# Kernel tuning notes

Hardware: AMD Instinct MI355X
Metric: run time of the kernel (lower is better)

Reference implementation:

```python
import jax, jax.numpy as jnp
import numpy as np

B, S, H, D = 2, 512, 64, 64   # batch, seq_len, head_dim, d_v=d_k
DT = 0.01                      # uniform measurement time step
NU, DELTA, ETA = 0.5, 1.0, 1.0


def _cmat(k, dout, din, scale):
    kr, ki = jax.random.split(k)
    return jnp.stack([jax.random.normal(kr, (dout, din)),
                      jax.random.normal(ki, (dout, din))]) * scale


def _cmm(W, b, X):
    """Complex matmul + bias. W:(2,O,I), b:(2,O,1), X:(B,2,S,I) -> (B,2,S,O)."""
    Yr = X[:, 0] @ W[0].T - X[:, 1] @ W[1].T + b[0].T
    Yi = X[:, 0] @ W[1].T + X[:, 1] @ W[0].T + b[1].T
    return jnp.stack([Yr, Yi], axis=1)


def _chad(K, V):
    """Complex hadamard of kernel K:(2,Si,Sj,D) with V:(B,2,Sj,D) -> (B,2,Si,Sj,D)."""
    Vr, Vi = V[:, 0, None], V[:, 1, None]           # (B,1,Sj,D)
    return jnp.stack([K[0][None] * Vr - K[1][None] * Vi,
                      K[0][None] * Vi + K[1][None] * Vr], axis=1)


def setup_inputs() -> dict:
    key = jax.random.key(0)
    ks = jax.random.split(key, 20)
    sc = 1.0 / np.sqrt(2 * H)
    t = jnp.arange(S + 1, dtype=jnp.float32) * DT
    return {
        "X_q": jax.random.normal(ks[0], (B, 2, S, H), jnp.float32),
        "X_k": jax.random.normal(ks[1], (B, 2, S, H), jnp.float32),
        "X_v": jax.random.normal(ks[2], (B, 2, S, H), jnp.float32),
        "t_measure_all": jnp.tile(t[None], (B, 1)),
        "lambda1": jnp.stack([jax.random.normal(ks[3], (D // 2, 1)),
                              jax.random.normal(ks[4], (D // 2, 1))]),
        "lam_Omega_sqrt": jax.random.normal(ks[5], (1, D, 1)) / np.sqrt(D),
        "lam_Omega0_sqrt": jax.random.normal(ks[6], (1, D, 1)) / np.sqrt(D),
        "lam_Gamma_sqrt": jax.random.normal(ks[7], (1, D, 1)) / np.sqrt(D),
        "lam_C": jnp.ones((1, D, 1), jnp.float32),
        "W_q": _cmat(ks[8], D, H, sc), "W_k": _cmat(ks[9], D, H, sc),
        "W_v": _cmat(ks[10], D, H, sc), "W_p": _cmat(ks[11], H, D, sc),
        "W_e": _cmat(ks[12], H, D, sc),
        "b_q": _cmat(ks[13], D, 1, sc), "b_k": _cmat(ks[14], D, 1, sc),
        "b_v": _cmat(ks[15], D, 1, sc), "b_p": _cmat(ks[16], H, 1, sc),
        "b_e": _cmat(ks[17], H, 1, sc),
    }


def reference(X_q, X_k, X_v, t_measure_all, lambda1, lam_Omega_sqrt,
              lam_Omega0_sqrt, lam_Gamma_sqrt, lam_C, W_q, W_k, W_v, W_p, W_e,
              b_q, b_k, b_v, b_p, b_e):
    # Stable conjugate-pair eigenvalues lambda_h (real<0) from lambda1 (2, D/2, 1)
    lr = -jnp.abs(lambda1[0, :, 0])
    li = lambda1[1, :, 0]
    real = jnp.concatenate([lr, lr])        # (D,)
    imag = jnp.concatenate([li, -li])       # (D,)
    Om = (lam_Omega_sqrt ** 2)[0, :, 0]
    Om0 = (lam_Omega0_sqrt ** 2)[0, :, 0]
    Gam = (lam_Gamma_sqrt ** 2)[0, :, 0]
    C = lam_C[0, :, 0]

    # Complex QKV projections
    Q = _cmm(W_q, b_q, X_q)
    Kk = _cmm(W_k, b_k, X_k)
    V = _cmm(W_v, b_v, X_v)

    # Pairwise propagation kernel exp(lambda * (t_i - t_j))
    t = t_measure_all[0, :-1]                       # (S,)
    dt = t[:, None] - t[None, :]                    # (S,S)
    decay = jnp.exp(real * dt[:, :, None])
    ph = imag * dt[:, :, None]
    Kexp = jnp.stack([decay * jnp.cos(ph), decay * jnp.sin(ph)])  # (2,S,S,D)

    # Kalman steady-state precision: propagated variance + measurement noise
    exp2 = jnp.exp((2.0 * real) * jnp.abs(dt)[:, :, None])        # (S,S,D)
    var = exp2 * Om0 + Om * (exp2 - 1.0) / (2.0 * real)
    P = 1.0 / (C ** 2 * var + Gam)                                # (S,S,D)

    # Estimates (propagated values) and residuals (query vs propagated key)
    Xhat = _chad(Kexp, V)                           # (B,2,S,S,D)
    Khat = _chad(Kexp, Kk)
    R = Q[:, :, :, None, :] - C * Khat              # (B,2,S,S,D)

    maha = P * (R[:, 0] ** 2 + R[:, 1] ** 2)        # (B,S,S,D)
    denom = 1.0 + NU * jnp.sum(maha, axis=-1, keepdims=True)
    mask = jnp.tril(jnp.ones((S, S), X_q.dtype))[:, :, None]
    A = (P / denom) * mask
    Xhat = Xhat * mask
    Qij = A / jnp.sum(A, axis=2, keepdims=True)     # normalize over j
    est_v = jnp.sum(Qij[:, None] * Xhat, axis=3)    # (B,2,S,D)

    est = _cmm(W_e, b_e, est_v)

    # One-step prediction in eigenbasis
    dtl = t_measure_all[:, -1] - t_measure_all[:, -2]   # (B,)
    dr = jnp.exp(real * dtl[:, None])
    pph = imag * dtl[:, None]
    mr, mi = dr * jnp.cos(pph), dr * jnp.sin(pph)       # (B,D)
    pr = mr[:, None] * est_v[:, 0] - mi[:, None] * est_v[:, 1]
    pi = mr[:, None] * est_v[:, 1] + mi[:, None] * est_v[:, 0]
    pred = _cmm(W_p, b_p, jnp.stack([pr, pi], axis=1))

    out = DELTA * pred + ETA * est
    return (est, out, Qij, Xhat, jnp.stack([real, imag]))
```

## Files before the change

### kernel.cpp

```cpp
#include <hip/hip_runtime.h>
#include <math.h>

#define SQ 512
#define NU_C 0.5f

typedef float fvec4 __attribute__((ext_vector_type(4)));

#define EST_OFF   0
#define OUT_OFF   131072
#define QIJ_OFF   262144
#define XHAT_OFF  33816576
#define LAM_OFF   100925440

#define WQ_OFF  0
#define WK_OFF  131072
#define WV_OFF  262144
#define WEV_OFF 393216

__global__ __launch_bounds__(256) void proj_kernel(
    const float* __restrict__ Xq, const float* __restrict__ Xk, const float* __restrict__ Xv,
    const float* __restrict__ Wq, const float* __restrict__ Wk, const float* __restrict__ Wv,
    const float* __restrict__ bq, const float* __restrict__ bk, const float* __restrict__ bv,
    float* __restrict__ ws)
{
    const int TILE = 16;
    __shared__ float WT0[64 * 65];
    __shared__ float WT1[64 * 65];
    __shared__ float XT[2 * TILE * 64];

    int t   = threadIdx.x;
    int blk = blockIdx.x;
    int p   = blk >> 6;
    int sub = blk & 63;
    int b   = sub >> 5;
    int s0  = (sub & 31) * TILE;

    const float* Xs[3]   = {Xq, Xk, Xv};
    const float* Wsrc[3] = {Wq, Wk, Wv};
    const float* bs[3]   = {bq, bk, bv};
    float* dst[3] = {ws + WQ_OFF, ws + WK_OFF, ws + WV_OFF};

    const float* W = Wsrc[p];
    for (int it = 0; it < 16; ++it) {
        int e = it * 256 + t;
        int dd = e >> 6, hw = e & 63;
        WT0[hw * 65 + dd] = W[e];
        WT1[hw * 65 + dd] = W[4096 + e];
    }
    const float* X = Xs[p];
    for (int it = 0; it < (2 * TILE * 64) / 256; ++it) {
        int e = it * 256 + t;
        int ri = e >> 10;
        int sl = (e >> 6) & (TILE - 1);
        int hw = e & 63;
        XT[e] = X[(size_t)(b * 2 + ri) * (SQ * 64) + (size_t)(s0 + sl) * 64 + hw];
    }
    __syncthreads();

    int dd = t & 63, sg = t >> 6;
    float b0 = bs[p][dd], b1 = bs[p][64 + dd];
    for (int sl = sg; sl < TILE; sl += 4) {
        float ar = b0, ai = b1;
        for (int h = 0; h < 64; ++h) {
            float xr = XT[sl * 64 + h];
            float xi = XT[TILE * 64 + sl * 64 + h];
            float w0 = WT0[h * 65 + dd];
            float w1 = WT1[h * 65 + dd];
            ar += xr * w0 - xi * w1;
            ai += xr * w1 + xi * w0;
        }
        float2 o; o.x = ar; o.y = ai;
        *(float2*)&dst[p][(size_t)((b * SQ + s0 + sl) * 64 + dd) * 2] = o;
    }
}

__global__ __launch_bounds__(512, 4) void main_kernel(
    const float* __restrict__ tm,
    const float* __restrict__ lam1,
    const float* __restrict__ lOm, const float* __restrict__ lOm0,
    const float* __restrict__ lGam, const float* __restrict__ lC,
    const float* __restrict__ ws,
    float* __restrict__ evw,
    float* __restrict__ out)
{
    __shared__ float t_lds[SQ];
    __shared__ float rden_l[2][SQ];
    __shared__ float red[8][2][3][64];

    int tid  = threadIdx.x;
    int lane = tid & 63;
    int wave = tid >> 6;
    int d = lane;
    int bx = (int)blockIdx.x;
    int i = (bx < 256) ? (SQ - 1 - bx) : (bx - 256);

    float l0 = lam1[d & 31];
    float l1 = lam1[32 + (d & 31)];
    float realv = -fabsf(l0);
    float imagv = (d < 32) ? l1 : -l1;
    float Om  = lOm[d]  * lOm[d];
    float Om0 = lOm0[d] * lOm0[d];
    float Gam = lGam[d] * lGam[d];
    float C   = lC[d];
    float C2  = C * C;
    float r2r = 1.0f / (2.0f * realv);
    float pA  = C2 * (Om0 + Om * r2r);
    float pB  = Gam - C2 * Om * r2r;

    for (int q = tid; q < SQ; q += 512) t_lds[q] = tm[q];
    __syncthreads();

    const float2* Kw = (const float2*)(ws + WK_OFF);
    const float2* Vw = (const float2*)(ws + WV_OFF);
    const float2* Qw = (const float2*)(ws + WQ_OFF);

    float ti = t_lds[i];
    float2 q0 = Qw[(0 * SQ + i) * 64 + d];
    float2 q1 = Qw[(1 * SQ + i) * 64 + d];
    float sA0 = 0, sXr0 = 0, sXi0 = 0, sA1 = 0, sXr1 = 0, sXi1 = 0;

    float* xh0 = out + XHAT_OFF + (size_t)(0 * SQ + i) * SQ * 64;
    float* xh1 = out + XHAT_OFF + (size_t)(1 * SQ + i) * SQ * 64;
    float* xh2 = out + XHAT_OFF + (size_t)(2 * SQ + i) * SQ * 64;
    float* xh3 = out + XHAT_OFF + (size_t)(3 * SQ + i) * SQ * 64;
    float* qij0 = out + QIJ_OFF + (size_t)(0 * SQ + i) * SQ * 64;
    float* qij1 = out + QIJ_OFF + (size_t)(1 * SQ + i) * SQ * 64;

    #pragma unroll 2
    for (int j = wave; j <= i; j += 8) {
        float dt = ti - t_lds[j];
        float e = __expf(realv * dt);
        float sph, cph;
        __sincosf(imagv * dt, &sph, &cph);
        float ar = e * cph, ai = e * sph;
        float e2 = e * e;
        float P = 1.0f / fmaf(e2, pA, pB);

        float2 k0 = Kw[(0 * SQ + j) * 64 + d];
        float2 v0 = Vw[(0 * SQ + j) * 64 + d];
        float2 k1 = Kw[(1 * SQ + j) * 64 + d];
        float2 v1 = Vw[(1 * SQ + j) * 64 + d];

        float xr0 = ar * v0.x - ai * v0.y, xi0 = ar * v0.y + ai * v0.x;
        float xr1 = ar * v1.x - ai * v1.y, xi1 = ar * v1.y + ai * v1.x;
        float khr0 = ar * k0.x - ai * k0.y, khi0 = ar * k0.y + ai * k0.x;
        float khr1 = ar * k1.x - ai * k1.y, khi1 = ar * k1.y + ai * k1.x;
        float Rr0 = q0.x - C * khr0, Ri0 = q0.y - C * khi0;
        float Rr1 = q1.x - C * khr1, Ri1 = q1.y - C * khi1;
        float m0 = P * fmaf(Rr0, Rr0, Ri0 * Ri0);
        float m1 = P * fmaf(Rr1, Rr1, Ri1 * Ri1);
        #pragma unroll
        for (int off = 32; off > 0; off >>= 1) {
            m0 += __shfl_xor(m0, off);
            m1 += __shfl_xor(m1, off);
        }
        float rd0 = 1.0f / (1.0f + NU_C * m0);
        float rd1 = 1.0f / (1.0f + NU_C * m1);
        float A0 = P * rd0, A1 = P * rd1;
        sA0 += A0; sXr0 = fmaf(A0, xr0, sXr0); sXi0 = fmaf(A0, xi0, sXi0);
        sA1 += A1; sXr1 = fmaf(A1, xr1, sXr1); sXi1 = fmaf(A1, xi1, sXi1);

        size_t jb = (size_t)j * 64 + d;
        __builtin_nontemporal_store(xr0, xh0 + jb);
        __builtin_nontemporal_store(xi0, xh1 + jb);
        __builtin_nontemporal_store(xr1, xh2 + jb);
        __builtin_nontemporal_store(xi1, xh3 + jb);
        if (lane == 0) { rden_l[0][j] = rd0; rden_l[1][j] = rd1; }
    }
    red[wave][0][0][d] = sA0; red[wave][0][1][d] = sXr0; red[wave][0][2][d] = sXi0;
    red[wave][1][0][d] = sA1; red[wave][1][1][d] = sXr1; red[wave][1][2][d] = sXi1;
    __syncthreads();

    float tA0 = 0, tXr0 = 0, tXi0 = 0, tA1 = 0, tXr1 = 0, tXi1 = 0;
    #pragma unroll
    for (int w = 0; w < 8; ++w) {
        tA0 += red[w][0][0][d]; tXr0 += red[w][0][1][d]; tXi0 += red[w][0][2][d];
        tA1 += red[w][1][0][d]; tXr1 += red[w][1][1][d]; tXi1 += red[w][1][2][d];
    }
    float rs0 = 1.0f / tA0, rs1 = 1.0f / tA1;
    if (wave == 0) {
        float2 ev0; ev0.x = tXr0 * rs0; ev0.y = tXi0 * rs0;
        float2 ev1; ev1.x = tXr1 * rs1; ev1.y = tXi1 * rs1;
        *(float2*)&evw[(size_t)((0 * SQ + i) * 64 + d) * 2] = ev0;
        *(float2*)&evw[(size_t)((1 * SQ + i) * 64 + d) * 2] = ev1;
    }

    #pragma unroll 2
    for (int j = wave; j <= i; j += 8) {
        float dt = ti - t_lds[j];
        float e2 = __expf(2.0f * realv * dt);
        float P = 1.0f / fmaf(e2, pA, pB);
        float qv0 = P * rden_l[0][j] * rs0;
        float qv1 = P * rden_l[1][j] * rs1;
        size_t jb = (size_t)j * 64 + d;
        __builtin_nontemporal_store(qv0, qij0 + jb);
        __builtin_nontemporal_store(qv1, qij1 + jb);
    }

    int nz4 = ((SQ - 1 - i) * 64) >> 2;
    if (nz4 > 0) {
        fvec4 z = {0.f, 0.f, 0.f, 0.f};
        size_t zb = (size_t)(i + 1) * 64;
        float* regs[6] = {qij0 + zb, qij1 + zb, xh0 + zb, xh1 + zb, xh2 + zb, xh3 + zb};
        for (int r6 = 0; r6 < 6; ++r6) {
            float* p4 = regs[r6];
            for (int k4 = tid; k4 < nz4; k4 += 512)
                __builtin_nontemporal_store(z, (fvec4*)(p4 + (size_t)k4 * 4));
        }
    }
}

__global__ __launch_bounds__(256) void epi_kernel(
    const float* __restrict__ tm,
    const float* __restrict__ lam1,
    const float* __restrict__ We, const float* __restrict__ be,
    const float* __restrict__ Wp, const float* __restrict__ bp,
    const float* __restrict__ evw,
    float* __restrict__ out)
{
    const int TILE = 8;
    __shared__ float WT0[64 * 65];
    __shared__ float WT1[64 * 65];
    __shared__ float EVr[TILE * 64];
    __shared__ float EVi[TILE * 64];
    __shared__ float mr_s[64], mi_s[64];

    int t = threadIdx.x;
    int blk = blockIdx.x;
    int b = blk >> 6;
    int s0 = (blk & 63) * TILE;

    if (blk == 0 && t < 128) {
        int dd = t & 63;
        float l0 = lam1[dd & 31];
        float l1 = lam1[32 + (dd & 31)];
        float v = (t < 64) ? -fabsf(l0) : ((dd < 32) ? l1 : -l1);
        out[LAM_OFF + t] = v;
    }
    if (t < 64) {
        int dd = t;
        float l0 = lam1[dd & 31];
        float l1 = lam1[32 + (dd & 31)];
        float realv = -fabsf(l0);
        float imagv = (dd < 32) ? l1 : -l1;
        float dtl = tm[b * (SQ + 1) + SQ] - tm[b * (SQ + 1) + SQ - 1];
        float e = __expf(realv * dtl);
        float s, c; __sincosf(imagv * dtl, &s, &c);
        mr_s[dd] = e * c; mi_s[dd] = e * s;
    }
    {
        const float* src = evw + (size_t)(b * SQ + s0) * 128;
        for (int it = 0; it < (TILE * 128) / 256; ++it) {
            int e = it * 256 + t;
            float v = src[e];
            int sl = e >> 7, dd = (e >> 1) & 63, ri = e & 1;
            if (ri == 0) EVr[sl * 64 + dd] = v; else EVi[sl * 64 + dd] = v;
        }
    }
    for (int it = 0; it < 16; ++it) {
        int e = it * 256 + t;
        int hw = e >> 6, dd = e & 63;
        WT0[dd * 65 + hw] = We[e];
        WT1[dd * 65 + hw] = We[4096 + e];
    }
    __syncthreads();

    int h = t & 63, sg = t >> 6;
    float estr[2], esti[2];
    float be0 = be[h], be1 = be[64 + h];
    #pragma unroll
    for (int k = 0; k < 2; ++k) {
        int sl = sg + k * 4;
        float ar = be0, ai = be1;
        for (int dd = 0; dd < 64; ++dd) {
            float er = EVr[sl * 64 + dd], ei = EVi[sl * 64 + dd];
            float w0 = WT0[dd * 65 + h], w1 = WT1[dd * 65 + h];
            ar += er * w0 - ei * w1;
            ai += er * w1 + ei * w0;
        }
        estr[k] = ar; esti[k] = ai;
        out[EST_OFF + (size_t)((b * 2 + 0) * SQ + s0 + sl) * 64 + h] = ar;
        out[EST_OFF + (size_t)((b * 2 + 1) * SQ + s0 + sl) * 64 + h] = ai;
    }
    __syncthreads();
    for (int it = 0; it < 16; ++it) {
        int e = it * 256 + t;
        int hw = e >> 6, dd = e & 63;
        WT0[dd * 65 + hw] = Wp[e];
        WT1[dd * 65 + hw] = Wp[4096 + e];
    }
    __syncthreads();
    float bp0 = bp[h], bp1 = bp[64 + h];
    #pragma unroll
    for (int k = 0; k < 2; ++k) {
        int sl = sg + k * 4;
        float ar = bp0, ai = bp1;
        for (int dd = 0; dd < 64; ++dd) {
            float er = EVr[sl * 64 + dd], ei = EVi[sl * 64 + dd];
            float pr = mr_s[dd] * er - mi_s[dd] * ei;
            float pi = mr_s[dd] * ei + mi_s[dd] * er;
            float w0 = WT0[dd * 65 + h], w1 = WT1[dd * 65 + h];
            ar += pr * w0 - pi * w1;
            ai += pr * w1 + pi * w0;
        }
        out[OUT_OFF + (size_t)((b * 2 + 0) * SQ + s0 + sl) * 64 + h] = ar + estr[k];
        out[OUT_OFF + (size_t)((b * 2 + 1) * SQ + s0 + sl) * 64 + h] = ai + esti[k];
    }
}

extern "C" void kernel_launch(void* const* d_in, const int* in_sizes, int n_in,
                              void* d_out, int out_size, void* d_ws, size_t ws_size,
                              hipStream_t stream)
{
    const float* Xq   = (const float*)d_in[0];
    const float* Xk   = (const float*)d_in[1];
    const float* Xv   = (const float*)d_in[2];
    const float* tm   = (const float*)d_in[3];
    const float* lam1 = (const float*)d_in[4];
    const float* lOm  = (const float*)d_in[5];
    const float* lOm0 = (const float*)d_in[6];
    const float* lGam = (const float*)d_in[7];
    const float* lC   = (const float*)d_in[8];
    const float* Wq   = (const float*)d_in[9];
    const float* Wk   = (const float*)d_in[10];
    const float* Wv   = (const float*)d_in[11];
    const float* Wp   = (const float*)d_in[12];
    const float* We   = (const float*)d_in[13];
    const float* bq   = (const float*)d_in[14];
    const float* bk   = (const float*)d_in[15];
    const float* bv   = (const float*)d_in[16];
    const float* bp   = (const float*)d_in[17];
    const float* be   = (const float*)d_in[18];
    float* out = (float*)d_out;
    float* ws  = (float*)d_ws;

    proj_kernel<<<192, 256, 0, stream>>>(Xq, Xk, Xv, Wq, Wk, Wv, bq, bk, bv, ws);
    main_kernel<<<512, 512, 0, stream>>>(tm, lam1, lOm, lOm0, lGam, lC, ws, ws + WEV_OFF, out);
    epi_kernel<<<128, 256, 0, stream>>>(tm, lam1, We, be, Wp, bp, ws + WEV_OFF, out);
}
```

Measured before the change: 113.5 us.

## Process two j rows per wave with two d lanes per thread

Remaps the main kernel so each wave handles two key rows j at once (half-waves of 32 lanes), with each lane covering two adjacent d values. This allows 16-byte vector loads of K/V/Q and 8-byte vector stores of Xhat/Qij, and shortens the cross-lane reduction to 5 shuffle steps. It also moves the final reduction to wave 0 and broadcasts the reciprocal sums through shared memory. The costs are an extra barrier, a per-iteration bounds check with possible half-wave idling, and higher register pressure.

Result: no change. 112.3 us (median of 2 runs) (-1.1%).

```diff
diff --git a/kernel.cpp b/kernel.cpp
--- a/kernel.cpp
+++ b/kernel.cpp
@@ -5,6 +5,7 @@
 #define NU_C 0.5f
 
 typedef float fvec4 __attribute__((ext_vector_type(4)));
+typedef float fvec2 __attribute__((ext_vector_type(2)));
 
 #define EST_OFF   0
 #define OUT_OFF   131072
@@ -86,38 +87,45 @@
     __shared__ float t_lds[SQ];
     __shared__ float rden_l[2][SQ];
     __shared__ float red[8][2][3][64];
+    __shared__ float rs_l[2][64];
 
     int tid  = threadIdx.x;
     int lane = tid & 63;
     int wave = tid >> 6;
-    int d = lane;
+    int q    = lane & 31;
+    int h2   = lane >> 5;
+    int d0   = 2 * q, d1 = 2 * q + 1;
     int bx = (int)blockIdx.x;
     int i = (bx < 256) ? (SQ - 1 - bx) : (bx - 256);
 
-    float l0 = lam1[d & 31];
-    float l1 = lam1[32 + (d & 31)];
-    float realv = -fabsf(l0);
-    float imagv = (d < 32) ? l1 : -l1;
-    float Om  = lOm[d]  * lOm[d];
-    float Om0 = lOm0[d] * lOm0[d];
-    float Gam = lGam[d] * lGam[d];
-    float C   = lC[d];
-    float C2  = C * C;
-    float r2r = 1.0f / (2.0f * realv);
-    float pA  = C2 * (Om0 + Om * r2r);
-    float pB  = Gam - C2 * Om * r2r;
-
-    for (int q = tid; q < SQ; q += 512) t_lds[q] = tm[q];
-    __syncthreads();
-
-    const float2* Kw = (const float2*)(ws + WK_OFF);
-    const float2* Vw = (const float2*)(ws + WV_OFF);
-    const float2* Qw = (const float2*)(ws + WQ_OFF);
+    float la0 = lam1[d0 & 31], lb0 = lam1[32 + (d0 & 31)];
+    float la1 = lam1[d1 & 31], lb1 = lam1[32 + (d1 & 31)];
+    float rv0 = -fabsf(la0),  rv1 = -fabsf(la1);
+    float iv0 = (d0 < 32) ? lb0 : -lb0;
+    float iv1 = (d1 < 32) ? lb1 : -lb1;
+    float Om_0 = lOm[d0] * lOm[d0],   Om_1 = lOm[d1] * lOm[d1];
+    float Oo_0 = lOm0[d0] * lOm0[d0], Oo_1 = lOm0[d1] * lOm0[d1];
+    float Gm_0 = lGam[d0] * lGam[d0], Gm_1 = lGam[d1] * lGam[d1];
+    float C_0 = lC[d0], C_1 = lC[d1];
+    float r2r0 = 1.0f / (2.0f * rv0), r2r1 = 1.0f / (2.0f * rv1);
+    float pA0 = C_0 * C_0 * (Oo_0 + Om_0 * r2r0);
+    float pB0 = Gm_0 - C_0 * C_0 * Om_0 * r2r0;
+    float pA1 = C_1 * C_1 * (Oo_1 + Om_1 * r2r1);
+    float pB1 = Gm_1 - C_1 * C_1 * Om_1 * r2r1;
+
+    for (int s = tid; s < SQ; s += 512) t_lds[s] = tm[s];
+    __syncthreads();
+
+    const fvec4* Kw4 = (const fvec4*)(ws + WK_OFF);
+    const fvec4* Vw4 = (const fvec4*)(ws + WV_OFF);
+    const fvec4* Qw4 = (const fvec4*)(ws + WQ_OFF);
 
     float ti = t_lds[i];
-    float2 q0 = Qw[(0 * SQ + i) * 64 + d];
-    float2 q1 = Qw[(1 * SQ + i) * 64 + d];
-    float sA0 = 0, sXr0 = 0, sXi0 = 0, sA1 = 0, sXr1 = 0, sXi1 = 0;
+    fvec4 qb0 = Qw4[(size_t)(0 * SQ + i) * 32 + q];
+    fvec4 qb1 = Qw4[(size_t)(1 * SQ + i) * 32 + q];
+
+    float sA00 = 0, sA01 = 0, sXr00 = 0, sXr01 = 0, sXi00 = 0, sXi01 = 0;
+    float sA10 = 0, sA11 = 0, sXr10 = 0, sXr11 = 0, sXi10 = 0, sXi11 = 0;
 
     float* xh0 = out + XHAT_OFF + (size_t)(0 * SQ + i) * SQ * 64;
     float* xh1 = out + XHAT_OFF + (size_t)(1 * SQ + i) * SQ * 64;
@@ -127,74 +135,114 @@
     float* qij1 = out + QIJ_OFF + (size_t)(1 * SQ + i) * SQ * 64;
 
     #pragma unroll 2
-    for (int j = wave; j <= i; j += 8) {
-        float dt = ti - t_lds[j];
-        float e = __expf(realv * dt);
-        float sph, cph;
-        __sincosf(imagv * dt, &sph, &cph);
-        float ar = e * cph, ai = e * sph;
-        float e2 = e * e;
-        float P = 1.0f / fmaf(e2, pA, pB);
-
-        float2 k0 = Kw[(0 * SQ + j) * 64 + d];
-        float2 v0 = Vw[(0 * SQ + j) * 64 + d];
-        float2 k1 = Kw[(1 * SQ + j) * 64 + d];
-        float2 v1 = Vw[(1 * SQ + j) * 64 + d];
-
-        float xr0 = ar * v0.x - ai * v0.y, xi0 = ar * v0.y + ai * v0.x;
-        float xr1 = ar * v1.x - ai * v1.y, xi1 = ar * v1.y + ai * v1.x;
-        float khr0 = ar * k0.x - ai * k0.y, khi0 = ar * k0.y + ai * k0.x;
-        float khr1 = ar * k1.x - ai * k1.y, khi1 = ar * k1.y + ai * k1.x;
-        float Rr0 = q0.x - C * khr0, Ri0 = q0.y - C * khi0;
-        float Rr1 = q1.x - C * khr1, Ri1 = q1.y - C * khi1;
-        float m0 = P * fmaf(Rr0, Rr0, Ri0 * Ri0);
-        float m1 = P * fmaf(Rr1, Rr1, Ri1 * Ri1);
+    for (int j0 = 2 * wave; j0 <= i; j0 += 16) {
+        int j = j0 + h2;
+        if (j <= i) {
+            float dt = ti - t_lds[j];
+            float e_0 = __expf(rv0 * dt);
+            float e_1 = __expf(rv1 * dt);
+            float s_0, c_0, s_1, c_1;
+            __sincosf(iv0 * dt, &s_0, &c_0);
+            __sincosf(iv1 * dt, &s_1, &c_1);
+            float ar0 = e_0 * c_0, ai0 = e_0 * s_0;
+            float ar1 = e_1 * c_1, ai1 = e_1 * s_1;
+            float P_0 = 1.0f / fmaf(e_0 * e_0, pA0, pB0);
+            float P_1 = 1.0f / fmaf(e_1 * e_1, pA1, pB1);
+
+            fvec4 k0 = Kw4[(size_t)(0 * SQ + j) * 32 + q];
+            fvec4 v0 = Vw4[(size_t)(0 * SQ + j) * 32 + q];
+            fvec4 k1 = Kw4[(size_t)(1 * SQ + j) * 32 + q];
+            fvec4 v1 = Vw4[(size_t)(1 * SQ + j) * 32 + q];
+
+            float xr00 = ar0 * v0[0] - ai0 * v0[1], xi00 = ar0 * v0[1] + ai0 * v0[0];
+            float xr01 = ar1 * v0[2] - ai1 * v0[3], xi01 = ar1 * v0[3] + ai1 * v0[2];
+            float kr00 = ar0 * k0[0] - ai0 * k0[1], ki00 = ar0 * k0[1] + ai0 * k0[0];
+            float kr01 = ar1 * k0[2] - ai1 * k0[3], ki01 = ar1 * k0[3] + ai1 * k0[2];
+            float Rr00 = qb0[0] - C_0 * kr00, Ri00 = qb0[1] - C_0 * ki00;
+            float Rr01 = qb0[2] - C_1 * kr01, Ri01 = qb0[3] - C_1 * ki01;
+            float xr10 = ar0 * v1[0] - ai0 * v1[1], xi10 = ar0 * v1[1] + ai0 * v1[0];
+            float xr11 = ar1 * v1[2] - ai1 * v1[3], xi11 = ar1 * v1[3] + ai1 * v1[2];
+            float kr10 = ar0 * k1[0] - ai0 * k1[1], ki10 = ar0 * k1[1] + ai0 * k1[0];
+            float kr11 = ar1 * k1[2] - ai1 * k1[3], ki11 = ar1 * k1[3] + ai1 * k1[2];
+            float Rr10 = qb1[0] - C_0 * kr10, Ri10 = qb1[1] - C_0 * ki10;
+            float Rr11 = qb1[2] - C_1 * kr11, Ri11 = qb1[3] - C_1 * ki11;
+
+            float m0 = P_0 * fmaf(Rr00, Rr00, Ri00 * Ri00) + P_1 * fmaf(Rr01, Rr01, Ri01 * Ri01);
+            float m1 = P_0 * fmaf(Rr10, Rr10, Ri10 * Ri10) + P_1 * fmaf(Rr11, Rr11, Ri11 * Ri11);
+            #pragma unroll
+            for (int off = 16; off > 0; off >>= 1) {
+                m0 += __shfl_xor(m0, off);
+                m1 += __shfl_xor(m1, off);
+            }
+            float rdb0 = 1.0f / (1.0f + NU_C * m0);
+            float rdb1 = 1.0f / (1.0f + NU_C * m1);
+            float A00 = P_0 * rdb0, A01 = P_1 * rdb0;
+            float A10 = P_0 * rdb1, A11 = P_1 * rdb1;
+            sA00 += A00; sXr00 = fmaf(A00, xr00, sXr00); sXi00 = fmaf(A00, xi00, sXi00);
+            sA01 += A01; sXr01 = fmaf(A01, xr01, sXr01); sXi01 = fmaf(A01, xi01, sXi01);
+            sA10 += A10; sXr10 = fmaf(A10, xr10, sXr10); sXi10 = fmaf(A10, xi10, sXi10);
+            sA11 += A11; sXr11 = fmaf(A11, xr11, sXr11); sXi11 = fmaf(A11, xi11, sXi11);
+
+            size_t jb = (size_t)j * 64 + d0;
+            fvec2 w0v = {xr00, xr01}; __builtin_nontemporal_store(w0v, (fvec2*)(xh0 + jb));
+            fvec2 w1v = {xi00, xi01}; __builtin_nontemporal_store(w1v, (fvec2*)(xh1 + jb));
+            fvec2 w2v = {xr10, xr11}; __builtin_nontemporal_store(w2v, (fvec2*)(xh2 + jb));
+            fvec2 w3v = {xi10, xi11}; __builtin_nontemporal_store(w3v, (fvec2*)(xh3 + jb));
+            if (q == 0) { rden_l[0][j] = rdb0; rden_l[1][j] = rdb1; }
+        }
+    }
+
+    sA00 += __shfl_xor(sA00, 32); sXr00 += __shfl_xor(sXr00, 32); sXi00 += __shfl_xor(sXi00, 32);
+    sA01 += __shfl_xor(sA01, 32); sXr01 += __shfl_xor(sXr01, 32); sXi01 += __shfl_xor(sXi01, 32);
+    sA10 += __shfl_xor(sA10, 32); sXr10 += __shfl_xor(sXr10, 32); sXi10 += __shfl_xor(sXi10, 32);
+    sA11 += __shfl_xor(sA11, 32); sXr11 += __shfl_xor(sXr11, 32); sXi11 += __shfl_xor(sXi11, 32);
+    if (h2 == 0) {
+        fvec2 a0 = {sA00, sA01};  *(fvec2*)&red[wave][0][0][d0] = a0;
+        fvec2 x0 = {sXr00, sXr01}; *(fvec2*)&red[wave][0][1][d0] = x0;
+        fvec2 y0 = {sXi00, sXi01}; *(fvec2*)&red[wave][0][2][d0] = y0;
+        fvec2 a1 = {sA10, sA11};  *(fvec2*)&red[wave][1][0][d0] = a1;
+        fvec2 x1 = {sXr10, sXr11}; *(fvec2*)&red[wave][1][1][d0] = x1;
+        fvec2 y1 = {sXi10, sXi11}; *(fvec2*)&red[wave][1][2][d0] = y1;
+    }
+    __syncthreads();
+
+    if (wave == 0) {
+        int d = lane;
+        float tA0 = 0, tXr0 = 0, tXi0 = 0, tA1 = 0, tXr1 = 0, tXi1 = 0;
         #pragma unroll
-        for (int off = 32; off > 0; off >>= 1) {
-            m0 += __shfl_xor(m0, off);
-            m1 += __shfl_xor(m1, off);
-        }
-        float rd0 = 1.0f / (1.0f + NU_C * m0);
-        float rd1 = 1.0f / (1.0f + NU_C * m1);
-        float A0 = P * rd0, A1 = P * rd1;
-        sA0 += A0; sXr0 = fmaf(A0, xr0, sXr0); sXi0 = fmaf(A0, xi0, sXi0);
-        sA1 += A1; sXr1 = fmaf(A1, xr1, sXr1); sXi1 = fmaf(A1, xi1, sXi1);
-
-        size_t jb = (size_t)j * 64 + d;
-        __builtin_nontemporal_store(xr0, xh0 + jb);
-        __builtin_nontemporal_store(xi0, xh1 + jb);
-        __builtin_nontemporal_store(xr1, xh2 + jb);
-        __builtin_nontemporal_store(xi1, xh3 + jb);
-        if (lane == 0) { rden_l[0][j] = rd0; rden_l[1][j] = rd1; }
-    }
-    red[wave][0][0][d] = sA0; red[wave][0][1][d] = sXr0; red[wave][0][2][d] = sXi0;
-    red[wave][1][0][d] = sA1; red[wave][1][1][d] = sXr1; red[wave][1][2][d] = sXi1;
-    __syncthreads();
-
-    float tA0 = 0, tXr0 = 0, tXi0 = 0, tA1 = 0, tXr1 = 0, tXi1 = 0;
-    #pragma unroll
-    for (int w = 0; w < 8; ++w) {
-        tA0 += red[w][0][0][d]; tXr0 += red[w][0][1][d]; tXi0 += red[w][0][2][d];
-        tA1 += red[w][1][0][d]; tXr1 += red[w][1][1][d]; tXi1 += red[w][1][2][d];
-    }
-    float rs0 = 1.0f / tA0, rs1 = 1.0f / tA1;
-    if (wave == 0) {
+        for (int w = 0; w < 8; ++w) {
+            tA0 += red[w][0][0][d]; tXr0 += red[w][0][1][d]; tXi0 += red[w][0][2][d];
+            tA1 += red[w][1][0][d]; tXr1 += red[w][1][1][d]; tXi1 += red[w][1][2][d];
+        }
+        float rs0 = 1.0f / tA0, rs1 = 1.0f / tA1;
+        rs_l[0][d] = rs0; rs_l[1][d] = rs1;
         float2 ev0; ev0.x = tXr0 * rs0; ev0.y = tXi0 * rs0;
         float2 ev1; ev1.x = tXr1 * rs1; ev1.y = tXi1 * rs1;
         *(float2*)&evw[(size_t)((0 * SQ + i) * 64 + d) * 2] = ev0;
         *(float2*)&evw[(size_t)((1 * SQ + i) * 64 + d) * 2] = ev1;
     }
+    __syncthreads();
+
+    float rs00 = rs_l[0][d0], rs01 = rs_l[0][d1];
+    float rs10 = rs_l[1][d0], rs11 = rs_l[1][d1];
 
     #pragma unroll 2
-    for (int j = wave; j <= i; j += 8) {
-        float dt = ti - t_lds[j];
-        float e2 = __expf(2.0f * realv * dt);
-        float P = 1.0f / fmaf(e2, pA, pB);
-        float qv0 = P * rden_l[0][j] * rs0;
-        float qv1 = P * rden_l[1][j] * rs1;
-        size_t jb = (size_t)j * 64 + d;
-        __builtin_nontemporal_store(qv0, qij0 + jb);
-        __builtin_nontemporal_store(qv1, qij1 + jb);
+    for (int j0 = 2 * wave; j0 <= i; j0 += 16) {
+        int j = j0 + h2;
+        if (j <= i) {
+            float dt = ti - t_lds[j];
+            float e2_0 = __expf(2.0f * rv0 * dt);
+            float e2_1 = __expf(2.0f * rv1 * dt);
+            float P_0 = 1.0f / fmaf(e2_0, pA0, pB0);
+            float P_1 = 1.0f / fmaf(e2_1, pA1, pB1);
+            float rdb0 = rden_l[0][j];
+            float rdb1 = rden_l[1][j];
+            size_t jb = (size_t)j * 64 + d0;
+            fvec2 q0v = {P_0 * rdb0 * rs00, P_1 * rdb0 * rs01};
+            fvec2 q1v = {P_0 * rdb1 * rs10, P_1 * rdb1 * rs11};
+            __builtin_nontemporal_store(q0v, (fvec2*)(qij0 + jb));
+            __builtin_nontemporal_store(q1v, (fvec2*)(qij1 + jb));
+        }
     }
 
     int nz4 = ((SQ - 1 - i) * 64) >> 2;
```
